# Kernel tuning notes

Measured on AMD Instinct MI355X. Metric: run time of the kernel, lower is better.

## Reference

```python
import jax, jax.numpy as jnp
import numpy as np

N = 100000      # nodes
E = 1600000     # edges
IN = 64         # in_feats
H = 64          # h_feats
L = 4           # num_conv_layers
FC = 2          # num_fc_layers
G = 512         # num graphs in batch
EPS = 1e-5      # BatchNorm eps


def _bn(x, g, b):
    # training-mode BatchNorm1d: batch stats (biased variance), affine
    m = x.mean(axis=0)
    v = x.var(axis=0)
    return (x - m) * jax.lax.rsqrt(v + EPS) * g + b


def setup_inputs() -> dict:
    key = jax.random.key(0)
    ks = jax.random.split(key, 12)
    x = jax.random.normal(ks[0], (N, IN), jnp.float32)
    edge_index = jax.random.randint(ks[1], (2, E), 0, N)
    batch = jnp.sort(jax.random.randint(ks[2], (N,), 0, G))
    s_in = 1.0 / np.sqrt(IN)
    s_h = 1.0 / np.sqrt(H)
    return {
        "x": x,
        "edge_index": edge_index,
        "batch": batch,
        "bn_feat_g": jnp.ones((IN,), jnp.float32),
        "bn_feat_b": jnp.zeros((IN,), jnp.float32),
        "lin_feat_W": jax.random.normal(ks[3], (IN, H), jnp.float32) * s_in,
        "lin_feat_b": jnp.zeros((H,), jnp.float32),
        "bn_conv_g": jnp.ones((L, H), jnp.float32),
        "bn_conv_b": jnp.zeros((L, H), jnp.float32),
        "conv_W": jax.random.normal(ks[4], (L, H, H), jnp.float32) * s_h,
        "conv_b": jnp.zeros((L, H), jnp.float32),
        "bn_fc_g": jnp.ones((FC, H), jnp.float32),
        "bn_fc_b": jnp.zeros((FC, H), jnp.float32),
        "fc_W": jax.random.normal(ks[5], (FC, H, H), jnp.float32) * s_h,
        "fc_b": jnp.zeros((FC, H), jnp.float32),
        "bn_hid_g": jnp.ones((H,), jnp.float32),
        "bn_hid_b": jnp.zeros((H,), jnp.float32),
    }


def reference(x, edge_index, batch, bn_feat_g, bn_feat_b, lin_feat_W, lin_feat_b,
              bn_conv_g, bn_conv_b, conv_W, conv_b, bn_fc_g, bn_fc_b, fc_W, fc_b,
              bn_hid_g, bn_hid_b):
    # --- GCN symmetric normalization with self-loops (computed once) ---
    loop = jnp.arange(N)
    src = jnp.concatenate([edge_index[0], loop])   # source j
    dst = jnp.concatenate([edge_index[1], loop])   # target i
    deg = jax.ops.segment_sum(jnp.ones((E + N,), x.dtype), dst, num_segments=N)
    dinv = jnp.where(deg > 0, 1.0, 0.0) / jnp.sqrt(jnp.where(deg > 0, deg, 1.0))
    norm = dinv[src] * dinv[dst]                   # [E+N]

    # --- stem ---
    h = _bn(x, bn_feat_g, bn_feat_b)
    h = jax.nn.relu(h @ lin_feat_W + lin_feat_b)

    # --- stacked GCNConv + BN + ReLU + residual ---
    for i in range(L):
        h_ = _bn(h, bn_conv_g[i], bn_conv_b[i])
        m = h_ @ conv_W[i]                                    # [N,H]
        agg = jax.ops.segment_sum(norm[:, None] * m[src], dst, num_segments=N)
        h = h + jax.nn.relu(agg + conv_b[i])                  # residual=True

    # --- global add pool over graphs ---
    h = jax.ops.segment_sum(h, batch, num_segments=G)         # [G,H]

    # --- fc head ---
    for i in range(FC):
        h_ = _bn(h, bn_fc_g[i], bn_fc_b[i])
        h = jax.nn.relu(h_ @ fc_W[i] + fc_b[i])

    return _bn(h, bn_hid_g, bn_hid_b)
```

## Files before the change

### kernel.cpp

```cpp
#include <hip/hip_runtime.h>
#include <hip/hip_fp16.h>

#define NN 100000
#define EE 1600000
#define GG 512
#define NB ((NN + 255) / 256)
#define SORT_CAP 48

__global__ void deg_kernel(const int* __restrict__ ei, int* __restrict__ cnt, int E_) {
    int e = blockIdx.x * 256 + threadIdx.x;
    if (e < E_) atomicAdd(&cnt[ei[E_ + e]], 1);
}

__global__ void dinv_kernel(const int* __restrict__ cnt, float* __restrict__ dinv, int n) {
    int i = blockIdx.x * 256 + threadIdx.x;
    if (i < n) dinv[i] = rsqrtf((float)cnt[i] + 1.0f);
}

__global__ void blocksum(const int* __restrict__ cnt, int* __restrict__ bsum) {
    __shared__ int sh[256];
    int i = blockIdx.x * 256 + threadIdx.x;
    sh[threadIdx.x] = (i < NN) ? cnt[i] : 0;
    __syncthreads();
    for (int o = 128; o > 0; o >>= 1) {
        if (threadIdx.x < o) sh[threadIdx.x] += sh[threadIdx.x + o];
        __syncthreads();
    }
    if (threadIdx.x == 0) bsum[blockIdx.x] = sh[0];
}

__global__ void scan_bsum(int* __restrict__ bsum, int nb) {
    __shared__ int sh[512];
    int t = threadIdx.x;
    int v = (t < nb) ? bsum[t] : 0;
    int orig = v;
    sh[t] = v;
    __syncthreads();
    for (int o = 1; o < 512; o <<= 1) {
        int add = (t >= o) ? sh[t - o] : 0;
        __syncthreads();
        sh[t] += add;
        __syncthreads();
    }
    if (t < nb) bsum[t] = sh[t] - orig;
}

__global__ void scan_final(const int* __restrict__ cnt, const int* __restrict__ boff,
                           int* __restrict__ row_ptr, int* __restrict__ cursor) {
    __shared__ int sh[256];
    int i = blockIdx.x * 256 + threadIdx.x;
    int v = (i < NN) ? cnt[i] : 0;
    int orig = v;
    sh[threadIdx.x] = v;
    __syncthreads();
    for (int o = 1; o < 256; o <<= 1) {
        int add = (threadIdx.x >= o) ? sh[threadIdx.x - o] : 0;
        __syncthreads();
        sh[threadIdx.x] += add;
        __syncthreads();
    }
    if (i < NN) {
        int ex = boff[blockIdx.x] + sh[threadIdx.x] - orig;
        row_ptr[i] = ex;
        cursor[i] = ex;
    }
    if (i == 0) row_ptr[NN] = EE;
}

__global__ void fill_csr(const int* __restrict__ ei, const float* __restrict__ dinv,
                         int* __restrict__ cursor, int* __restrict__ csr_src,
                         float* __restrict__ csr_norm, int E_) {
    int e = blockIdx.x * 256 + threadIdx.x;
    if (e < E_) {
        int s = ei[e], d = ei[E_ + e];
        int pos = atomicAdd(&cursor[d], 1);
        csr_src[pos] = s;
        csr_norm[pos] = dinv[s] * dinv[d];
    }
}

__global__ __launch_bounds__(128) void sort_adj(const int* __restrict__ row_ptr,
                                                int* __restrict__ csr_src,
                                                float* __restrict__ csr_norm) {
    __shared__ unsigned long long buf[SORT_CAP * 128];
    int t = threadIdx.x;
    int i = blockIdx.x * 128 + t;
    if (i >= NN) return;
    int e0 = row_ptr[i], e1 = row_ptr[i + 1];
    int d = e1 - e0;
    if (d < 2 || d > SORT_CAP) return;
    for (int j = 0; j < d; j++) {
        unsigned long long k = ((unsigned long long)(unsigned)csr_src[e0 + j] << 32)
                             | (unsigned long long)__float_as_uint(csr_norm[e0 + j]);
        buf[j * 128 + t] = k;
    }
    for (int j = 1; j < d; j++) {
        unsigned long long key = buf[j * 128 + t];
        int k = j - 1;
        while (k >= 0 && buf[k * 128 + t] > key) {
            buf[(k + 1) * 128 + t] = buf[k * 128 + t];
            k--;
        }
        buf[(k + 1) * 128 + t] = key;
    }
    for (int j = 0; j < d; j++) {
        unsigned long long k = buf[j * 128 + t];
        csr_src[e0 + j] = (int)(k >> 32);
        csr_norm[e0 + j] = __uint_as_float((unsigned)k);
    }
}

__global__ void colstats(const float* __restrict__ A, int nrows, float* __restrict__ stats) {
    __shared__ float ssum[4][64];
    __shared__ float ssq[4][64];
    int tid = threadIdx.x;
    int col = tid & 63, rg = tid >> 6;
    float s = 0.f, q = 0.f;
    for (int r = blockIdx.x * 4 + rg; r < nrows; r += gridDim.x * 4) {
        float v = A[r * 64 + col];
        s += v;
        q = fmaf(v, v, q);
    }
    ssum[rg][col] = s; ssq[rg][col] = q;
    __syncthreads();
    if (tid < 64) {
        float ts = ssum[0][tid] + ssum[1][tid] + ssum[2][tid] + ssum[3][tid];
        float tq = ssq[0][tid] + ssq[1][tid] + ssq[2][tid] + ssq[3][tid];
        atomicAdd(&stats[tid], ts);
        atomicAdd(&stats[64 + tid], tq);
    }
}

__global__ void prep(const float* __restrict__ stats, float count,
                     const float* __restrict__ g, const float* __restrict__ b,
                     const float* __restrict__ W, const float* __restrict__ basebias,
                     float* __restrict__ Wp, float* __restrict__ bp) {
    int j = threadIdx.x;
    float acc = basebias ? basebias[j] : 0.f;
    for (int k = 0; k < 64; k++) {
        float mu  = stats[k] / count;
        float var = fmaxf(stats[64 + k] / count - mu * mu, 0.f);
        float rstd = rsqrtf(var + 1e-5f);
        float a = rstd * g[k];
        float w = W[k * 64 + j];
        Wp[k * 64 + j] = a * w;
        acc = fmaf(b[k] - mu * a, w, acc);
    }
    bp[j] = acc;
}

__global__ __launch_bounds__(256) void gemm64(const float* __restrict__ A,
                                              const float* __restrict__ Wp,
                                              const float* __restrict__ bp,
                                              float* __restrict__ C,
                                              __half* __restrict__ C16,
                                              int nrows, int dorelu,
                                              float* __restrict__ stats) {
    __shared__ float Ws[64 * 64];
    __shared__ float As[64 * 64];
    __shared__ float ssh[256];
    __shared__ float qsh[256];
    int tid = threadIdx.x;
    int row0 = blockIdx.x * 64;
    for (int i = tid; i < 4096; i += 256) {
        Ws[i] = Wp[i];
        int r = row0 + (i >> 6);
        As[i] = (r < nrows) ? A[row0 * 64 + i] : 0.f;
    }
    __syncthreads();
    int col = tid & 63;
    int rg = tid >> 6;
    float bcol = bp[col];
    float s = 0.f, q = 0.f;
    for (int rr = rg; rr < 64; rr += 4) {
        int r = row0 + rr;
        if (r >= nrows) break;
        float acc = bcol;
#pragma unroll
        for (int k = 0; k < 64; k++) acc = fmaf(As[rr * 64 + k], Ws[k * 64 + col], acc);
        float v = dorelu ? fmaxf(acc, 0.f) : acc;
        if (C)   C[r * 64 + col] = v;
        if (C16) C16[r * 64 + col] = __float2half(v);
        s += v;
        q = fmaf(v, v, q);
    }
    if (stats) {
        ssh[tid] = s; qsh[tid] = q;
        __syncthreads();
        if (tid < 64) {
            float ts = ssh[tid] + ssh[64 + tid] + ssh[128 + tid] + ssh[192 + tid];
            float tq = qsh[tid] + qsh[64 + tid] + qsh[128 + tid] + qsh[192 + tid];
            atomicAdd(&stats[tid], ts);
            atomicAdd(&stats[64 + tid], tq);
        }
    }
}

__device__ __forceinline__ void row4(const __half* __restrict__ base, int cl,
                                     float& x, float& y, float& z, float& w) {
    uint2 raw = ((const uint2*)base)[cl];
    __half2 h01 = *reinterpret_cast<const __half2*>(&raw.x);
    __half2 h23 = *reinterpret_cast<const __half2*>(&raw.y);
    float2 f01 = __half22float2(h01);
    float2 f23 = __half22float2(h23);
    x = f01.x; y = f01.y; z = f23.x; w = f23.y;
}

__global__ __launch_bounds__(256) void gather(const int* __restrict__ row_ptr,
                                              const int* __restrict__ csr_src,
                                              const float* __restrict__ csr_norm,
                                              const float* __restrict__ dinv,
                                              const __half* __restrict__ m,
                                              float* __restrict__ h,
                                              const float* __restrict__ cb,
                                              float* __restrict__ stats,
                                              float* __restrict__ pooled,
                                              const int* __restrict__ batch,
                                              int writeH) {
    int tid = threadIdx.x;
    int ng = tid >> 4;
    int cl = tid & 15;
    const float4* cb4 = (const float4*)cb;
    float4 cbv = cb4[cl];
    float sx = 0.f, sy = 0.f, sz = 0.f, sw = 0.f;
    float qx = 0.f, qy = 0.f, qz = 0.f, qw = 0.f;
    for (int i = blockIdx.x * 16 + ng; i < NN; i += gridDim.x * 16) {
        float di = dinv[i];
        float mx, my, mz, mw;
        row4(m + (size_t)i * 64, cl, mx, my, mz, mw);
        float d2 = di * di;
        float ax = d2 * mx, ay = d2 * my, az = d2 * mz, aw = d2 * mw;
        int e0 = row_ptr[i], e1 = row_ptr[i + 1];
        int e = e0;
        for (; e + 3 < e1; e += 4) {
            int s0 = csr_src[e + 0];
            int s1 = csr_src[e + 1];
            int s2 = csr_src[e + 2];
            int s3 = csr_src[e + 3];
            float w0 = csr_norm[e + 0];
            float w1 = csr_norm[e + 1];
            float w2 = csr_norm[e + 2];
            float w3 = csr_norm[e + 3];
            float x0, y0, z0, w0v, x1, y1, z1, w1v, x2, y2, z2, w2v, x3, y3, z3, w3v;
            row4(m + (size_t)s0 * 64, cl, x0, y0, z0, w0v);
            row4(m + (size_t)s1 * 64, cl, x1, y1, z1, w1v);
            row4(m + (size_t)s2 * 64, cl, x2, y2, z2, w2v);
            row4(m + (size_t)s3 * 64, cl, x3, y3, z3, w3v);
            ax = fmaf(w0, x0, ax); ay = fmaf(w0, y0, ay);
            az = fmaf(w0, z0, az); aw = fmaf(w0, w0v, aw);
            ax = fmaf(w1, x1, ax); ay = fmaf(w1, y1, ay);
            az = fmaf(w1, z1, az); aw = fmaf(w1, w1v, aw);
            ax = fmaf(w2, x2, ax); ay = fmaf(w2, y2, ay);
            az = fmaf(w2, z2, az); aw = fmaf(w2, w2v, aw);
            ax = fmaf(w3, x3, ax); ay = fmaf(w3, y3, ay);
            az = fmaf(w3, z3, az); aw = fmaf(w3, w3v, aw);
        }
        for (; e < e1; e++) {
            int s = csr_src[e];
            float w = csr_norm[e];
            float xs, ys, zs, wsv;
            row4(m + (size_t)s * 64, cl, xs, ys, zs, wsv);
            ax = fmaf(w, xs, ax);
            ay = fmaf(w, ys, ay);
            az = fmaf(w, zs, az);
            aw = fmaf(w, wsv, aw);
        }
        float4 hb = ((const float4*)(h + (size_t)i * 64))[cl];
        float nx = hb.x + fmaxf(ax + cbv.x, 0.f);
        float ny = hb.y + fmaxf(ay + cbv.y, 0.f);
        float nz = hb.z + fmaxf(az + cbv.z, 0.f);
        float nw = hb.w + fmaxf(aw + cbv.w, 0.f);
        if (writeH) {
            float4 o; o.x = nx; o.y = ny; o.z = nz; o.w = nw;
            ((float4*)(h + (size_t)i * 64))[cl] = o;
        }
        if (stats) {
            sx += nx; sy += ny; sz += nz; sw += nw;
            qx = fmaf(nx, nx, qx); qy = fmaf(ny, ny, qy);
            qz = fmaf(nz, nz, qz); qw = fmaf(nw, nw, qw);
        }
        if (pooled) {
            int g = batch[i];
            float* p = pooled + g * 64 + cl * 4;
            atomicAdd(p + 0, nx);
            atomicAdd(p + 1, ny);
            atomicAdd(p + 2, nz);
            atomicAdd(p + 3, nw);
        }
    }
    if (stats) {
        __shared__ float rs[256 * 4];
        __shared__ float rq[256 * 4];
        rs[tid * 4 + 0] = sx; rs[tid * 4 + 1] = sy; rs[tid * 4 + 2] = sz; rs[tid * 4 + 3] = sw;
        rq[tid * 4 + 0] = qx; rq[tid * 4 + 1] = qy; rq[tid * 4 + 2] = qz; rq[tid * 4 + 3] = qw;
        __syncthreads();
        if (tid < 64) {
            int cl2 = tid >> 2, k = tid & 3;
            float a = 0.f, b = 0.f;
            for (int g = 0; g < 16; g++) {
                a += rs[(g * 16 + cl2) * 4 + k];
                b += rq[(g * 16 + cl2) * 4 + k];
            }
            atomicAdd(&stats[tid], a);
            atomicAdd(&stats[64 + tid], b);
        }
    }
}

__global__ void bn_apply(const float* __restrict__ A, const float* __restrict__ stats, float count,
                         const float* __restrict__ g, const float* __restrict__ b,
                         float* __restrict__ out, int total) {
    int idx = blockIdx.x * 256 + threadIdx.x;
    if (idx < total) {
        int j = idx & 63;
        float mu  = stats[j] / count;
        float var = fmaxf(stats[64 + j] / count - mu * mu, 0.f);
        float rstd = rsqrtf(var + 1e-5f);
        out[idx] = (A[idx] - mu) * rstd * g[j] + b[j];
    }
}

extern "C" void kernel_launch(void* const* d_in, const int* in_sizes, int n_in,
                              void* d_out, int out_size, void* d_ws, size_t ws_size,
                              hipStream_t stream) {
    const float* x     = (const float*)d_in[0];
    const int*   ei    = (const int*)d_in[1];
    const int*   batch = (const int*)d_in[2];
    const float* bnfg  = (const float*)d_in[3];
    const float* bnfb  = (const float*)d_in[4];
    const float* linW  = (const float*)d_in[5];
    const float* linb  = (const float*)d_in[6];
    const float* bncg  = (const float*)d_in[7];
    const float* bncb  = (const float*)d_in[8];
    const float* convW = (const float*)d_in[9];
    const float* convb = (const float*)d_in[10];
    const float* bnfcg = (const float*)d_in[11];
    const float* bnfcb = (const float*)d_in[12];
    const float* fcW   = (const float*)d_in[13];
    const float* fcb   = (const float*)d_in[14];
    const float* bnhg  = (const float*)d_in[15];
    const float* bnhb  = (const float*)d_in[16];

    const int N64 = NN * 64;
    float* ws = (float*)d_ws;
    size_t o = 0;
    int*   cnt      = (int*)(ws + o);   o += 100352;
    float* dinv     = ws + o;           o += 100352;
    int*   row_ptr  = (int*)(ws + o);   o += 100352;
    int*   cursor   = (int*)(ws + o);   o += 100352;
    int*   bsum     = (int*)(ws + o);   o += 512;
    int*   csr_src  = (int*)(ws + o);   o += EE;
    float* csr_norm = ws + o;           o += EE;
    float* h        = ws + o;           o += N64;
    __half* m16     = (__half*)(ws + o); o += N64 / 2;
    float* statsA   = ws + o;           o += 128;
    float* statsB   = ws + o;           o += 128;
    float* Wp       = ws + o;           o += 4096;
    float* bp       = ws + o;           o += 64;
    float* pa       = ws + o;           o += GG * 64;
    float* pb       = ws + o;           o += GG * 64;

    hipMemsetAsync(cnt, 0, NN * sizeof(int), stream);
    deg_kernel<<<(EE + 255) / 256, 256, 0, stream>>>(ei, cnt, EE);
    dinv_kernel<<<NB, 256, 0, stream>>>(cnt, dinv, NN);
    blocksum<<<NB, 256, 0, stream>>>(cnt, bsum);
    scan_bsum<<<1, 512, 0, stream>>>(bsum, NB);
    scan_final<<<NB, 256, 0, stream>>>(cnt, bsum, row_ptr, cursor);
    fill_csr<<<(EE + 255) / 256, 256, 0, stream>>>(ei, dinv, cursor, csr_src, csr_norm, EE);
    sort_adj<<<(NN + 127) / 128, 128, 0, stream>>>(row_ptr, csr_src, csr_norm);

    hipMemsetAsync(statsA, 0, 512, stream);
    colstats<<<256, 256, 0, stream>>>(x, NN, statsA);
    prep<<<1, 64, 0, stream>>>(statsA, (float)NN, bnfg, bnfb, linW, linb, Wp, bp);
    hipMemsetAsync(statsB, 0, 512, stream);
    gemm64<<<(NN + 63) / 64, 256, 0, stream>>>(x, Wp, bp, h, nullptr, NN, 1, statsB);

    hipMemsetAsync(pa, 0, GG * 64 * sizeof(float), stream);
    float* cur = statsB; float* nxt = statsA;
    for (int l = 0; l < 4; l++) {
        prep<<<1, 64, 0, stream>>>(cur, (float)NN, bncg + 64 * l, bncb + 64 * l,
                                   convW + 4096 * l, nullptr, Wp, bp);
        gemm64<<<(NN + 63) / 64, 256, 0, stream>>>(h, Wp, bp, nullptr, m16, NN, 0, nullptr);
        if (l < 3) {
            hipMemsetAsync(nxt, 0, 512, stream);
            gather<<<2048, 256, 0, stream>>>(row_ptr, csr_src, csr_norm, dinv, m16, h,
                                             convb + 64 * l, nxt, nullptr, batch, 1);
        } else {
            gather<<<2048, 256, 0, stream>>>(row_ptr, csr_src, csr_norm, dinv, m16, h,
                                             convb + 64 * l, nullptr, pa, batch, 0);
        }
        float* t = cur; cur = nxt; nxt = t;
    }

    float* pin = pa; float* pout = pb;
    for (int i = 0; i < 2; i++) {
        hipMemsetAsync(statsA, 0, 512, stream);
        colstats<<<8, 256, 0, stream>>>(pin, GG, statsA);
        prep<<<1, 64, 0, stream>>>(statsA, (float)GG, bnfcg + 64 * i, bnfcb + 64 * i,
                                   fcW + 4096 * i, fcb + 64 * i, Wp, bp);
        gemm64<<<(GG + 63) / 64, 256, 0, stream>>>(pin, Wp, bp, pout, nullptr, GG, 1, nullptr);
        float* t = pin; pin = pout; pout = t;
    }

    hipMemsetAsync(statsA, 0, 512, stream);
    colstats<<<8, 256, 0, stream>>>(pin, GG, statsA);
    bn_apply<<<(GG * 64 + 255) / 256, 256, 0, stream>>>(pin, statsA, (float)GG, bnhg, bnhb,
                                                        (float*)d_out, GG * 64);
}
```

Before: 1.213 ms.

## Slice gather by source-node range with block barriers for cache locality

```diff
diff --git a/kernel.cpp b/kernel.cpp
--- a/kernel.cpp
+++ b/kernel.cpp
@@ -6,6 +6,11 @@
 #define GG 512
 #define NB ((NN + 255) / 256)
 #define SORT_CAP 48
+
+#define GBLK 1280
+#define NPG 5
+#define NSLICE 8
+#define SLICE ((NN + NSLICE - 1) / NSLICE)
 
 __global__ void deg_kernel(const int* __restrict__ ei, int* __restrict__ cnt, int E_) {
     int e = blockIdx.x * 256 + threadIdx.x;
@@ -88,25 +93,40 @@
     if (i >= NN) return;
     int e0 = row_ptr[i], e1 = row_ptr[i + 1];
     int d = e1 - e0;
-    if (d < 2 || d > SORT_CAP) return;
-    for (int j = 0; j < d; j++) {
-        unsigned long long k = ((unsigned long long)(unsigned)csr_src[e0 + j] << 32)
-                             | (unsigned long long)__float_as_uint(csr_norm[e0 + j]);
-        buf[j * 128 + t] = k;
-    }
-    for (int j = 1; j < d; j++) {
-        unsigned long long key = buf[j * 128 + t];
-        int k = j - 1;
-        while (k >= 0 && buf[k * 128 + t] > key) {
-            buf[(k + 1) * 128 + t] = buf[k * 128 + t];
-            k--;
-        }
-        buf[(k + 1) * 128 + t] = key;
-    }
-    for (int j = 0; j < d; j++) {
-        unsigned long long k = buf[j * 128 + t];
-        csr_src[e0 + j] = (int)(k >> 32);
-        csr_norm[e0 + j] = __uint_as_float((unsigned)k);
+    if (d < 2) return;
+    if (d <= SORT_CAP) {
+        for (int j = 0; j < d; j++) {
+            unsigned long long k = ((unsigned long long)(unsigned)csr_src[e0 + j] << 32)
+                                 | (unsigned long long)__float_as_uint(csr_norm[e0 + j]);
+            buf[j * 128 + t] = k;
+        }
+        for (int j = 1; j < d; j++) {
+            unsigned long long key = buf[j * 128 + t];
+            int k = j - 1;
+            while (k >= 0 && buf[k * 128 + t] > key) {
+                buf[(k + 1) * 128 + t] = buf[k * 128 + t];
+                k--;
+            }
+            buf[(k + 1) * 128 + t] = key;
+        }
+        for (int j = 0; j < d; j++) {
+            unsigned long long k = buf[j * 128 + t];
+            csr_src[e0 + j] = (int)(k >> 32);
+            csr_norm[e0 + j] = __uint_as_float((unsigned)k);
+        }
+    } else {
+        for (int j = 1; j < d; j++) {
+            int ks = csr_src[e0 + j];
+            float kn = csr_norm[e0 + j];
+            int k = j - 1;
+            while (k >= 0 && csr_src[e0 + k] > ks) {
+                csr_src[e0 + k + 1] = csr_src[e0 + k];
+                csr_norm[e0 + k + 1] = csr_norm[e0 + k];
+                k--;
+            }
+            csr_src[e0 + k + 1] = ks;
+            csr_norm[e0 + k + 1] = kn;
+        }
     }
 }
 
@@ -222,54 +242,85 @@
     int cl = tid & 15;
     const float4* cb4 = (const float4*)cb;
     float4 cbv = cb4[cl];
+    int base = blockIdx.x * (16 * NPG);
+
+    int cur[NPG], eend[NPG];
+    float ax[NPG], ay[NPG], az[NPG], aw_[NPG];
+#pragma unroll
+    for (int n = 0; n < NPG; n++) {
+        int i = base + n * 16 + ng;
+        if (i < NN) {
+            float di = dinv[i];
+            float d2 = di * di;
+            float mx, my, mz, mw;
+            row4(m + (size_t)i * 64, cl, mx, my, mz, mw);
+            ax[n] = d2 * mx; ay[n] = d2 * my; az[n] = d2 * mz; aw_[n] = d2 * mw;
+            cur[n] = row_ptr[i];
+            eend[n] = row_ptr[i + 1];
+        } else {
+            ax[n] = ay[n] = az[n] = aw_[n] = 0.f;
+            cur[n] = 0; eend[n] = 0;
+        }
+    }
+
+    for (int s = 0; s < NSLICE; s++) {
+        int hi = (s + 1) * SLICE;
+#pragma unroll
+        for (int n = 0; n < NPG; n++) {
+            int e = cur[n], e1 = eend[n];
+            int eseg = e;
+            while (eseg < e1 && csr_src[eseg] < hi) eseg++;
+            float AX = ax[n], AY = ay[n], AZ = az[n], AW = aw_[n];
+            for (; e + 3 < eseg; e += 4) {
+                int s0 = csr_src[e + 0];
+                int s1 = csr_src[e + 1];
+                int s2 = csr_src[e + 2];
+                int s3 = csr_src[e + 3];
+                float w0 = csr_norm[e + 0];
+                float w1 = csr_norm[e + 1];
+                float w2 = csr_norm[e + 2];
+                float w3 = csr_norm[e + 3];
+                float x0, y0, z0, w0v, x1, y1, z1, w1v, x2, y2, z2, w2v, x3, y3, z3, w3v;
+                row4(m + (size_t)s0 * 64, cl, x0, y0, z0, w0v);
+                row4(m + (size_t)s1 * 64, cl, x1, y1, z1, w1v);
+                row4(m + (size_t)s2 * 64, cl, x2, y2, z2, w2v);
+                row4(m + (size_t)s3 * 64, cl, x3, y3, z3, w3v);
+                AX = fmaf(w0, x0, AX); AY = fmaf(w0, y0, AY);
+                AZ = fmaf(w0, z0, AZ); AW = fmaf(w0, w0v, AW);
+                AX = fmaf(w1, x1, AX); AY = fmaf(w1, y1, AY);
+                AZ = fmaf(w1, z1, AZ); AW = fmaf(w1, w1v, AW);
+                AX = fmaf(w2, x2, AX); AY = fmaf(w2, y2, AY);
+                AZ = fmaf(w2, z2, AZ); AW = fmaf(w2, w2v, AW);
+                AX = fmaf(w3, x3, AX); AY = fmaf(w3, y3, AY);
+                AZ = fmaf(w3, z3, AZ); AW = fmaf(w3, w3v, AW);
+            }
+            for (; e < eseg; e++) {
+                int sn = csr_src[e];
+                float w = csr_norm[e];
+                float xs, ys, zs, wsv;
+                row4(m + (size_t)sn * 64, cl, xs, ys, zs, wsv);
+                AX = fmaf(w, xs, AX);
+                AY = fmaf(w, ys, AY);
+                AZ = fmaf(w, zs, AZ);
+                AW = fmaf(w, wsv, AW);
+            }
+            ax[n] = AX; ay[n] = AY; az[n] = AZ; aw_[n] = AW;
+            cur[n] = eseg;
+        }
+        __syncthreads();
+    }
+
     float sx = 0.f, sy = 0.f, sz = 0.f, sw = 0.f;
     float qx = 0.f, qy = 0.f, qz = 0.f, qw = 0.f;
-    for (int i = blockIdx.x * 16 + ng; i < NN; i += gridDim.x * 16) {
-        float di = dinv[i];
-        float mx, my, mz, mw;
-        row4(m + (size_t)i * 64, cl, mx, my, mz, mw);
-        float d2 = di * di;
-        float ax = d2 * mx, ay = d2 * my, az = d2 * mz, aw = d2 * mw;
-        int e0 = row_ptr[i], e1 = row_ptr[i + 1];
-        int e = e0;
-        for (; e + 3 < e1; e += 4) {
-            int s0 = csr_src[e + 0];
-            int s1 = csr_src[e + 1];
-            int s2 = csr_src[e + 2];
-            int s3 = csr_src[e + 3];
-            float w0 = csr_norm[e + 0];
-            float w1 = csr_norm[e + 1];
-            float w2 = csr_norm[e + 2];
-            float w3 = csr_norm[e + 3];
-            float x0, y0, z0, w0v, x1, y1, z1, w1v, x2, y2, z2, w2v, x3, y3, z3, w3v;
-            row4(m + (size_t)s0 * 64, cl, x0, y0, z0, w0v);
-            row4(m + (size_t)s1 * 64, cl, x1, y1, z1, w1v);
-            row4(m + (size_t)s2 * 64, cl, x2, y2, z2, w2v);
-            row4(m + (size_t)s3 * 64, cl, x3, y3, z3, w3v);
-            ax = fmaf(w0, x0, ax); ay = fmaf(w0, y0, ay);
-            az = fmaf(w0, z0, az); aw = fmaf(w0, w0v, aw);
-            ax = fmaf(w1, x1, ax); ay = fmaf(w1, y1, ay);
-            az = fmaf(w1, z1, az); aw = fmaf(w1, w1v, aw);
-            ax = fmaf(w2, x2, ax); ay = fmaf(w2, y2, ay);
-            az = fmaf(w2, z2, az); aw = fmaf(w2, w2v, aw);
-            ax = fmaf(w3, x3, ax); ay = fmaf(w3, y3, ay);
-            az = fmaf(w3, z3, az); aw = fmaf(w3, w3v, aw);
-        }
-        for (; e < e1; e++) {
-            int s = csr_src[e];
-            float w = csr_norm[e];
-            float xs, ys, zs, wsv;
-            row4(m + (size_t)s * 64, cl, xs, ys, zs, wsv);
-            ax = fmaf(w, xs, ax);
-            ay = fmaf(w, ys, ay);
-            az = fmaf(w, zs, az);
-            aw = fmaf(w, wsv, aw);
-        }
+#pragma unroll
+    for (int n = 0; n < NPG; n++) {
+        int i = base + n * 16 + ng;
+        if (i >= NN) continue;
         float4 hb = ((const float4*)(h + (size_t)i * 64))[cl];
-        float nx = hb.x + fmaxf(ax + cbv.x, 0.f);
-        float ny = hb.y + fmaxf(ay + cbv.y, 0.f);
-        float nz = hb.z + fmaxf(az + cbv.z, 0.f);
-        float nw = hb.w + fmaxf(aw + cbv.w, 0.f);
+        float nx = hb.x + fmaxf(ax[n] + cbv.x, 0.f);
+        float ny = hb.y + fmaxf(ay[n] + cbv.y, 0.f);
+        float nz = hb.z + fmaxf(az[n] + cbv.z, 0.f);
+        float nw = hb.w + fmaxf(aw_[n] + cbv.w, 0.f);
         if (writeH) {
             float4 o; o.x = nx; o.y = ny; o.z = nz; o.w = nw;
             ((float4*)(h + (size_t)i * 64))[cl] = o;
@@ -383,10 +434,10 @@
         gemm64<<<(NN + 63) / 64, 256, 0, stream>>>(h, Wp, bp, nullptr, m16, NN, 0, nullptr);
         if (l < 3) {
             hipMemsetAsync(nxt, 0, 512, stream);
-            gather<<<2048, 256, 0, stream>>>(row_ptr, csr_src, csr_norm, dinv, m16, h,
+            gather<<<GBLK, 256, 0, stream>>>(row_ptr, csr_src, csr_norm, dinv, m16, h,
                                              convb + 64 * l, nxt, nullptr, batch, 1);
         } else {
-            gather<<<2048, 256, 0, stream>>>(row_ptr, csr_src, csr_norm, dinv, m16, h,
+            gather<<<GBLK, 256, 0, stream>>>(row_ptr, csr_src, csr_norm, dinv, m16, h,
                                              convb + 64 * l, nullptr, pa, batch, 0);
         }
         float* t = cur; cur = nxt; nxt = t;
```

Measured after the change: 1.606 ms. +32.5%, slower.
